# Optimization experiments

Hardware: AMD Instinct MI355X
Metric: run time of the kernel (lower is better)

## Reference

```python
import jax, jax.numpy as jnp
import numpy as np

MIN_HALF_LIFE = 15.0 / (24 * 60)   # days
MAX_HALF_LIFE = 274.0              # days
SECONDS_PER_DAY = 60.0 * 60.0 * 24.0
BASE = 2.0

B, N, T = 256, 512, 200


def setup_inputs() -> dict:
    key = jax.random.key(0)
    k0, k1, k2, k3, k4 = jax.random.split(key, 5)
    x0 = jax.random.uniform(k0, (B, N), dtype=jnp.float32)
    # sorted timestamps in seconds: cumulative gaps of up to ~2 days
    gaps = jax.random.uniform(k1, (B, T), dtype=jnp.float32, minval=60.0, maxval=2.0 * SECONDS_PER_DAY)
    t = jnp.cumsum(gaps, axis=-1)
    items = jax.random.randint(k2, (B, T), 0, N, dtype=jnp.int64)
    # history stats [N_total, N_success, N_failure], small non-negative counts
    stats = jax.random.randint(k3, (B, N, T, 3), 0, 20).astype(jnp.float32)
    theta = jax.random.normal(k4, (3,), dtype=jnp.float32) * 0.05  # xavier-ish scale for (1,3)
    return {"x0": x0, "t": t, "items": items, "stats": stats, "theta": theta}


def reference(x0, t, items, stats, theta):
    # train mode, stats precomputed -> loop over timesteps vectorizes exactly.
    feats = stats[:, :, :-1, :]                      # [B, N, T-1, 3] (step i uses stats at i-1)
    # half_life = hclip(base ** (feat @ theta))
    logits = jnp.einsum('bntk,k->bnt', feats, theta)  # [B, N, T-1]
    half_life = jnp.clip(jnp.exp2(logits), MIN_HALF_LIFE, MAX_HALF_LIFE)
    dt = jnp.diff(t, axis=-1)[:, None, :] / SECONDS_PER_DAY  # [B, 1, T-1] days (tiled over nodes)
    p_all = jax.nn.sigmoid(jnp.exp2(-dt / half_life))        # [B, N, T-1]
    # x_pred = [x0, p_all_1, ..., p_all_{T-1}] stacked on last axis -> [B, N, T]
    x_pred = jnp.concatenate([x0[..., None], p_all], axis=-1)
    # p_item: gather p_all at items[:, i] for i = 1..T-1
    idx = items[:, None, 1:]                                 # [B, 1, T-1]
    x_item_pred = jnp.take_along_axis(p_all, idx, axis=1)[:, 0, :]  # [B, T-1]
    return x_pred, x_item_pred, half_life
```

## Files before the change

kernel.cpp:

```cpp
#include <hip/hip_runtime.h>

constexpr int B = 256, N = 512, T = 200, TM1 = 199;
constexpr unsigned E_MAIN = (unsigned)B * N * TM1;
constexpr unsigned MAIN_BLOCKS = E_MAIN / 256;
constexpr unsigned ITEM_BLOCKS = ((unsigned)B * TM1) / 256;
constexpr float MIN_HL = 15.0f / (24.0f * 60.0f);
constexpr float MAX_HL = 274.0f;
constexpr float INV_SPD = 1.0f / 86400.0f;

struct F3 { float x, y, z; };

__device__ __forceinline__ float hl_of(float s0, float s1, float s2,
                                       float th0, float th1, float th2) {
    float logit = fmaf(s0, th0, fmaf(s1, th1, s2 * th2));
    return fminf(fmaxf(exp2f(logit), MIN_HL), MAX_HL);
}

__device__ __forceinline__ float p_of(float hl, float dt_days) {
    float z = exp2f(-dt_days / hl);
    return 1.0f / (1.0f + __expf(-z));
}

__global__ __launch_bounds__(256) void hlr_fused(
    const float* __restrict__ x0,
    const float* __restrict__ t,
    const int*   __restrict__ items,
    const float* __restrict__ stats,
    const float* __restrict__ theta,
    float* __restrict__ x_pred,
    float* __restrict__ x_item,
    float* __restrict__ half_life)
{
    const float th0 = theta[0], th1 = theta[1], th2 = theta[2];
    const unsigned bid = blockIdx.x;

    if (bid < MAIN_BLOCKS) {
        const unsigned e   = bid * 256u + threadIdx.x;
        const unsigned row = e / TM1;
        const unsigned j   = e - row * TM1;
        const unsigned b   = row >> 9;

        F3 s;
        __builtin_memcpy(&s, stats + (size_t)row * (T * 3) + (size_t)j * 3, sizeof(F3));

        const float* trow = t + (size_t)b * T;
        const float tj  = trow[j];
        const float tj1 = trow[j + 1];

        const float hl = hl_of(s.x, s.y, s.z, th0, th1, th2);
        const float p  = p_of(hl, (tj1 - tj) * INV_SPD);

        half_life[e] = hl;
        x_pred[(size_t)row * T + j + 1] = p;
        if (j == 0) x_pred[(size_t)row * T] = x0[row];
    } else {
        const int i = (int)(bid - MAIN_BLOCKS) * 256 + (int)threadIdx.x;
        const int b = i / TM1;
        const int j = i - b * TM1;
        const int n = items[(size_t)b * T + j + 1];

        F3 s;
        __builtin_memcpy(&s, stats + ((size_t)((size_t)b * N + n) * T + j) * 3, sizeof(F3));
        const float hl = hl_of(s.x, s.y, s.z, th0, th1, th2);
        const float dt = (t[(size_t)b * T + j + 1] - t[(size_t)b * T + j]) * INV_SPD;
        x_item[i] = p_of(hl, dt);
    }
}

extern "C" void kernel_launch(void* const* d_in, const int* in_sizes, int n_in,
                              void* d_out, int out_size, void* d_ws, size_t ws_size,
                              hipStream_t stream) {
    const float* x0    = (const float*)d_in[0];
    const float* t     = (const float*)d_in[1];
    const int*   items = (const int*)d_in[2];
    const float* stats = (const float*)d_in[3];
    const float* theta = (const float*)d_in[4];

    float* out = (float*)d_out;
    float* x_pred    = out;
    float* x_item    = out + (size_t)B * N * T;
    float* half_life = out + (size_t)B * N * T + (size_t)B * TM1;

    hlr_fused<<<MAIN_BLOCKS + ITEM_BLOCKS, 256, 0, stream>>>(
        x0, t, items, stats, theta, x_pred, x_item, half_life);
}
```

Baseline: 109.5 us.

## Map one block per row and stage outputs in LDS for vectorized nontemporal stores

Each block now handles one (b,n) row. It computes the 199 timesteps into shared memory, then writes x_pred and half_life as aligned float4 nontemporal stores, with scalar head and tail handling for half_life. This removes the per-element division by 199 and the misaligned scalar stores, and it avoids polluting the cache with streaming outputs. In exchange, 57 of the 256 threads in each block sit idle during compute, a barrier is added, and the grid becomes much larger with short-lived blocks.

New measurement: 112.8 us. 1.03x slower.

```diff
diff --git a/kernel.cpp b/kernel.cpp
--- a/kernel.cpp
+++ b/kernel.cpp
@@ -1,14 +1,13 @@
 #include <hip/hip_runtime.h>
 
+typedef float f32x4 __attribute__((ext_vector_type(4)));
+
 constexpr int B = 256, N = 512, T = 200, TM1 = 199;
-constexpr unsigned E_MAIN = (unsigned)B * N * TM1;
-constexpr unsigned MAIN_BLOCKS = E_MAIN / 256;
+constexpr unsigned ROWS = (unsigned)B * N;
 constexpr unsigned ITEM_BLOCKS = ((unsigned)B * TM1) / 256;
 constexpr float MIN_HL = 15.0f / (24.0f * 60.0f);
 constexpr float MAX_HL = 274.0f;
 constexpr float INV_SPD = 1.0f / 86400.0f;
-
-struct F3 { float x, y, z; };
 
 __device__ __forceinline__ float hl_of(float s0, float s1, float s2,
                                        float th0, float th1, float th2) {
@@ -34,36 +33,69 @@
     const float th0 = theta[0], th1 = theta[1], th2 = theta[2];
     const unsigned bid = blockIdx.x;
 
-    if (bid < MAIN_BLOCKS) {
-        const unsigned e   = bid * 256u + threadIdx.x;
-        const unsigned row = e / TM1;
-        const unsigned j   = e - row * TM1;
+    if (bid < ROWS) {
+        __shared__ float s_p[T];
+        __shared__ float s_h[T];
+
+        const unsigned row = bid;
         const unsigned b   = row >> 9;
+        const int j = (int)threadIdx.x;
 
-        F3 s;
-        __builtin_memcpy(&s, stats + (size_t)row * (T * 3) + (size_t)j * 3, sizeof(F3));
+        if (j < TM1) {
+            const float* sg = stats + (size_t)row * (T * 3) + (size_t)j * 3;
+            float s0, s1, s2;
+            __builtin_memcpy(&s0, sg,     4);
+            __builtin_memcpy(&s1, sg + 1, 4);
+            __builtin_memcpy(&s2, sg + 2, 4);
 
-        const float* trow = t + (size_t)b * T;
-        const float tj  = trow[j];
-        const float tj1 = trow[j + 1];
+            const float tj  = t[(size_t)b * T + j];
+            const float tj1 = t[(size_t)b * T + j + 1];
 
-        const float hl = hl_of(s.x, s.y, s.z, th0, th1, th2);
-        const float p  = p_of(hl, (tj1 - tj) * INV_SPD);
+            const float hl = hl_of(s0, s1, s2, th0, th1, th2);
+            const float p  = p_of(hl, (tj1 - tj) * INV_SPD);
 
-        half_life[e] = hl;
-        x_pred[(size_t)row * T + j + 1] = p;
-        if (j == 0) x_pred[(size_t)row * T] = x0[row];
+            s_p[j + 1] = p;
+            s_h[j]     = hl;
+            if (j == 0) s_p[0] = x0[row];
+        }
+        __syncthreads();
+
+        float* xp = x_pred + (size_t)row * T;
+        const unsigned k = threadIdx.x;
+        if (k < 50) {
+            f32x4 v = { s_p[4*k], s_p[4*k+1], s_p[4*k+2], s_p[4*k+3] };
+            __builtin_nontemporal_store(v, reinterpret_cast<f32x4*>(xp) + k);
+        }
+
+        const size_t base = (size_t)row * TM1;
+        const unsigned lead = (unsigned)((4 - (base & 3)) & 3);
+        if (k < lead)
+            __builtin_nontemporal_store(s_h[k], half_life + base + k);
+        const unsigned nvec = (TM1 - lead) >> 2;
+        if (k < nvec) {
+            const unsigned o = lead + 4*k;
+            f32x4 v = { s_h[o], s_h[o+1], s_h[o+2], s_h[o+3] };
+            __builtin_nontemporal_store(
+                v, reinterpret_cast<f32x4*>(half_life + base + lead) + k);
+        }
+        const unsigned done = lead + 4*nvec;
+        const unsigned tail = TM1 - done;
+        if (k < tail)
+            __builtin_nontemporal_store(s_h[done + k], half_life + base + done + k);
     } else {
-        const int i = (int)(bid - MAIN_BLOCKS) * 256 + (int)threadIdx.x;
+        const int i = (int)(bid - ROWS) * 256 + (int)threadIdx.x;
         const int b = i / TM1;
         const int j = i - b * TM1;
         const int n = items[(size_t)b * T + j + 1];
 
-        F3 s;
-        __builtin_memcpy(&s, stats + ((size_t)((size_t)b * N + n) * T + j) * 3, sizeof(F3));
-        const float hl = hl_of(s.x, s.y, s.z, th0, th1, th2);
+        const float* sg = stats + ((size_t)((size_t)b * N + n) * T + j) * 3;
+        float s0, s1, s2;
+        __builtin_memcpy(&s0, sg,     4);
+        __builtin_memcpy(&s1, sg + 1, 4);
+        __builtin_memcpy(&s2, sg + 2, 4);
+        const float hl = hl_of(s0, s1, s2, th0, th1, th2);
         const float dt = (t[(size_t)b * T + j + 1] - t[(size_t)b * T + j]) * INV_SPD;
-        x_item[i] = p_of(hl, dt);
+        __builtin_nontemporal_store(p_of(hl, dt), x_item + i);
     }
 }
 
@@ -81,6 +113,6 @@
     float* x_item    = out + (size_t)B * N * T;
     float* half_life = out + (size_t)B * N * T + (size_t)B * TM1;
 
-    hlr_fused<<<MAIN_BLOCKS + ITEM_BLOCKS, 256, 0, stream>>>(
+    hlr_fused<<<ROWS + ITEM_BLOCKS, 256, 0, stream>>>(
         x0, t, items, stats, theta, x_pred, x_item, half_life);
 }
```
